# Optimization experiments

Measured on AMD Instinct MI355X. Metric: run time of the kernel, lower is better.

The kernel has to match this reference:

```python
import jax, jax.numpy as jnp
import numpy as np

DIM = 2048
HEADS = 16
HDIM = DIM // HEADS  # 128
B = 1
F, HG, WG = 5, 20, 32
L = F * HG * WG  # 3200
EPS = 1e-6
MAXPOS = 1024
C = HDIM // 2  # 64 rotary pairs
S0 = C - 2 * (C // 3)  # 22 (frame band)
S1 = C // 3            # 21 (height band)


def _rope_tables():
    # Matches Wan rope_params: per-band inverse-freq tables, angle = pos * inv_freq.
    pos = np.arange(MAXPOS, dtype=np.float64)
    chunks = []
    for s in (S0, S1, S1):
        d = 2 * s
        inv = 1.0 / (10000.0 ** (np.arange(0, d, 2, dtype=np.float64) / d))
        chunks.append(np.outer(pos, inv))
    ang = np.concatenate(chunks, axis=1)  # [MAXPOS, C]
    return np.cos(ang).astype(np.float32), np.sin(ang).astype(np.float32)


def setup_inputs() -> dict:
    key = jax.random.key(0)
    ks = jax.random.split(key, 6)
    sc = 1.0 / np.sqrt(DIM)
    fc, fs = _rope_tables()
    return {
        'x': jax.random.normal(ks[0], (B, L, DIM), dtype=jnp.float32),
        'wq': jax.random.normal(ks[1], (DIM, DIM), dtype=jnp.float32) * sc,
        'bq': jnp.zeros((DIM,), jnp.float32),
        'wk': jax.random.normal(ks[2], (DIM, DIM), dtype=jnp.float32) * sc,
        'bk': jnp.zeros((DIM,), jnp.float32),
        'wv': jax.random.normal(ks[3], (DIM, DIM), dtype=jnp.float32) * sc,
        'bv': jnp.zeros((DIM,), jnp.float32),
        'wo': jax.random.normal(ks[4], (DIM, DIM), dtype=jnp.float32) * sc,
        'bo': jnp.zeros((DIM,), jnp.float32),
        'norm_q_w': jnp.ones((DIM,), jnp.float32),
        'norm_k_w': jnp.ones((DIM,), jnp.float32),
        'freqs_cos': jnp.asarray(fc),
        'freqs_sin': jnp.asarray(fs),
    }


def _grid_freqs(tab):
    # Split bands and broadcast over the (F, HG, WG) grid -> [L, C]
    bf, bh, bw = tab[:, :S0], tab[:, S0:S0 + S1], tab[:, S0 + S1:]
    gf = jnp.broadcast_to(bf[:F, None, None, :], (F, HG, WG, S0))
    gh = jnp.broadcast_to(bh[None, :HG, None, :], (F, HG, WG, S1))
    gw = jnp.broadcast_to(bw[None, None, :WG, :], (F, HG, WG, S1))
    return jnp.concatenate([gf, gh, gw], axis=-1).reshape(L, C)


def reference(x, wq, bq, wk, bk, wv, bv, wo, bo, norm_q_w, norm_k_w, freqs_cos, freqs_sin):
    def rms(t, w):
        return t * jax.lax.rsqrt(jnp.mean(t * t, axis=-1, keepdims=True) + EPS) * w

    q = rms(x @ wq.T + bq, norm_q_w).reshape(B, L, HEADS, HDIM)
    k = rms(x @ wk.T + bk, norm_k_w).reshape(B, L, HEADS, HDIM)
    v = (x @ wv.T + bv).reshape(B, L, HEADS, HDIM)

    fc = _grid_freqs(freqs_cos)  # [L, C]
    fs = _grid_freqs(freqs_sin)

    def rope(t):
        tr = t.reshape(B, L, HEADS, C, 2)
        xr, xi = tr[..., 0], tr[..., 1]
        c = fc[None, :, None, :]
        s = fs[None, :, None, :]
        return jnp.stack([xr * c - xi * s, xr * s + xi * c], axis=-1).reshape(B, L, HEADS, HDIM)

    q = rope(q)
    k = rope(k)

    scores = jnp.einsum('blhd,bmhd->bhlm', q, k) / jnp.sqrt(jnp.float32(HDIM))
    attn = jax.nn.softmax(scores, axis=-1)
    out = jnp.einsum('bhlm,bmhd->blhd', attn, v).reshape(B, L, DIM)
    return out @ wo.T + bo
```

## Files before the change

kernel.cpp:

```cpp
#include <hip/hip_runtime.h>

typedef unsigned short u16;
typedef unsigned int u32;
typedef __attribute__((ext_vector_type(4))) float f32x4;
typedef __attribute__((ext_vector_type(8))) short bf16x8;
typedef __attribute__((ext_vector_type(8))) u16 u16x8;
typedef __attribute__((ext_vector_type(4))) u16 u16x4;
typedef __attribute__((ext_vector_type(4))) u32 u32x4;

#define GLOB_AS __attribute__((address_space(1)))
#define LDS_AS  __attribute__((address_space(3)))

__device__ __forceinline__ void gload_lds16(const void* g, void* l) {
  __builtin_amdgcn_global_load_lds((const GLOB_AS void*)g, (LDS_AS void*)l, 16, 0, 0);
}

__device__ __forceinline__ u16 f2bf(float f) {
  u32 u = __builtin_bit_cast(u32, f);
  u += 0x7fffu + ((u >> 16) & 1u);
  return (u16)(u >> 16);
}

__device__ __forceinline__ float bf2f(u16 b) {
  u32 u = (u32)b << 16;
  return __builtin_bit_cast(float, u);
}

#define MFMA16(a, b, c) __builtin_amdgcn_mfma_f32_16x16x32_bf16(a, b, c, 0, 0, 0)

__global__ __launch_bounds__(256) void cast_all(const float* __restrict__ x,
                                                const float* __restrict__ wq,
                                                const float* __restrict__ wk,
                                                const float* __restrict__ wv,
                                                const float* __restrict__ wo,
                                                u16* __restrict__ xb, u16* __restrict__ wqb,
                                                u16* __restrict__ wkb, u16* __restrict__ wvb,
                                                u16* __restrict__ wob) {
  int i = blockIdx.x * 256 + threadIdx.x;
  const float* s;
  u16* d;
  int off;
  if (i < 819200)       { s = x;  d = xb;  off = i; }
  else if (i < 1343488) { s = wq; d = wqb; off = i - 819200; }
  else if (i < 1867776) { s = wk; d = wkb; off = i - 1343488; }
  else if (i < 2392064) { s = wv; d = wvb; off = i - 1867776; }
  else                  { s = wo; d = wob; off = i - 2392064; }
  f32x4 a = ((const f32x4*)s)[2 * off], b = ((const f32x4*)s)[2 * off + 1];
  u16x8 o;
  o[0] = f2bf(a[0]); o[1] = f2bf(a[1]); o[2] = f2bf(a[2]); o[3] = f2bf(a[3]);
  o[4] = f2bf(b[0]); o[5] = f2bf(b[1]); o[6] = f2bf(b[2]); o[7] = f2bf(b[3]);
  ((u16x8*)d)[off] = o;
}

#define GEMM_BODY(C_WRITE)                                                        \
  f32x4 acc[4][4] = {};                                                           \
  const u32 dstoff = wave * 2048 + lane * 8;       \
  int gsb = 0;                                                                    \
  const u16* Agp = Ag;                                                            \
  const u16* Bgp = Bg;                                                            \
  _Pragma("unroll") for (int pf = 0; pf < 2; ++pf) {                              \
    u16* ad = &As[gsb][0] + dstoff;                                               \
    u16* bd = &Bs[gsb][0] + dstoff;                                               \
    gload_lds16(Agp, ad);                                                         \
    gload_lds16(Agp + (size_t)8 * K + d4, ad + 512);                              \
    gload_lds16(Agp + (size_t)16 * K, ad + 1024);                                 \
    gload_lds16(Agp + (size_t)24 * K + d4, ad + 1536);                            \
    gload_lds16(Bgp, bd);                                                         \
    gload_lds16(Bgp + (size_t)8 * K + d4, bd + 512);                              \
    gload_lds16(Bgp + (size_t)16 * K, bd + 1024);                                 \
    gload_lds16(Bgp + (size_t)24 * K + d4, bd + 1536);                            \
    Agp += 64;                                                                    \
    Bgp += 64;                                                                    \
    gsb ^= 1;                                                                     \
  }                                                                               \
  for (int it = 0; it < 32; ++it) {                                               \
    const int buf = it & 1;                                                       \
    if (it < 31)                                                                  \
      asm volatile("s_waitcnt vmcnt(8)" ::: "memory");                            \
    else                                                                          \
      asm volatile("s_waitcnt vmcnt(0)" ::: "memory");                            \
    __builtin_amdgcn_s_barrier();                                                 \
    _Pragma("unroll") for (int kk = 0; kk < 64; kk += 32) {                       \
      bf16x8 af[4], bfr[4];                                                       \
      _Pragma("unroll") for (int mi = 0; mi < 4; mi++)                            \
          af[mi] = *(const bf16x8*)&As[buf][((wr + mi * 16 + li) >> 1) * 128 +    \
              ((((kk >> 3) + lg + 8 * (li & 1)) ^ (li >> 1)) * 8)];               \
      _Pragma("unroll") for (int ni = 0; ni < 4; ni++)                            \
          bfr[ni] = *(const bf16x8*)&Bs[buf][((wc + ni * 16 + li) >> 1) * 128 +   \
              ((((kk >> 3) + lg + 8 * (li & 1)) ^ (li >> 1)) * 8)];               \
      _Pragma("unroll") for (int mi = 0; mi < 4; mi++)                            \
          _Pragma("unroll") for (int ni = 0; ni < 4; ni++)                        \
              acc[mi][ni] = MFMA16(af[mi], bfr[ni], acc[mi][ni]);                 \
    }                                                                             \
    __builtin_amdgcn_s_barrier();                                                 \
    if (it <= 29) {                                                               \
      u16* ad = &As[gsb][0] + dstoff;                                             \
      u16* bd = &Bs[gsb][0] + dstoff;                                             \
      gload_lds16(Agp, ad);                                                       \
      gload_lds16(Agp + (size_t)8 * K + d4, ad + 512);                            \
      gload_lds16(Agp + (size_t)16 * K, ad + 1024);                               \
      gload_lds16(Agp + (size_t)24 * K + d4, ad + 1536);                          \
      gload_lds16(Bgp, bd);                                                       \
      gload_lds16(Bgp + (size_t)8 * K + d4, bd + 512);                            \
      gload_lds16(Bgp + (size_t)16 * K, bd + 1024);                               \
      gload_lds16(Bgp + (size_t)24 * K + d4, bd + 1536);                          \
      Agp += 64;                                                                  \
      Bgp += 64;                                                                  \
      gsb ^= 1;                                                                   \
    }                                                                             \
  }                                                                               \
  float bcol[4];                                                                  \
  _Pragma("unroll") for (int ni = 0; ni < 4; ni++)                                \
      bcol[ni] = bias[n0 + wc + ni * 16 + li];                                    \
  _Pragma("unroll") for (int mi = 0; mi < 4; mi++) {                              \
    _Pragma("unroll") for (int ni = 0; ni < 4; ni++) {                            \
      const int gm = m0 + wr + mi * 16 + lg * 4;                                  \
      const int gn = n0 + wc + ni * 16 + li;                                      \
      _Pragma("unroll") for (int r = 0; r < 4; r++) { C_WRITE; }                  \
    }                                                                             \
  }

#define GEMM_STAGE_SETUP()                                        \
  const int Wl = lane >> 4;                                       \
  const int sl = lane & 15;                                       \
  const int gsa = sl ^ Wl;                                        \
  const int d4 = ((((gsa & 7) ^ 4) - (gsa & 7)) * 8)

__global__ __launch_bounds__(256) void gemm_qkv(const u16* __restrict__ A,
                                                const u16* __restrict__ Bq,
                                                const u16* __restrict__ Bk,
                                                const u16* __restrict__ Bv,
                                                const float* __restrict__ bq,
                                                const float* __restrict__ bk,
                                                const float* __restrict__ bv,
                                                u16* __restrict__ Cq,
                                                u16* __restrict__ Ck,
                                                u16* __restrict__ Cv) {
  constexpr int K = 2048, N = 2048;
  __shared__ u16 As[2][128 * 64];
  __shared__ u16 Bs[2][128 * 64];
  const int tid = threadIdx.x;
  const int wave = tid >> 6, lane = tid & 63;
  const int lg = lane >> 4, li = lane & 15;
  const int lid = blockIdx.x + 25 * blockIdx.y;
  const int tile = (lid & 7) * 150 + (lid >> 3);
  const int bx = tile % 25, by = tile / 25;
  const int m0 = bx * 128;
  const int mat = by >> 4;
  const int n0 = (by & 15) * 128;
  const u16* B = (mat == 0) ? Bq : (mat == 1) ? Bk : Bv;
  const float* bias = (mat == 0) ? bq : (mat == 1) ? bk : bv;
  u16* C = (mat == 0) ? Cq : (mat == 1) ? Ck : Cv;
  const int wr = (wave >> 1) * 64, wc = (wave & 1) * 64;

  GEMM_STAGE_SETUP();
  const u16* Ag = A + (size_t)(m0 + wave * 32 + 2 * Wl + (sl >> 3)) * K + (gsa & 7) * 8;
  const u16* Bg = B + (size_t)(n0 + wave * 32 + 2 * Wl + (sl >> 3)) * K + (gsa & 7) * 8;

  GEMM_BODY(C[(size_t)(gm + r) * N + gn] = f2bf(acc[mi][ni][r] + bcol[ni]))
}

__global__ __launch_bounds__(256) void gemm_nt(const u16* __restrict__ A,
                                               const u16* __restrict__ B,
                                               const float* __restrict__ bias,
                                               float* __restrict__ C) {
  constexpr int K = 2048, N = 2048;
  __shared__ u16 As[2][128 * 64];
  __shared__ u16 Bs[2][128 * 64];
  const int tid = threadIdx.x;
  const int wave = tid >> 6, lane = tid & 63;
  const int lg = lane >> 4, li = lane & 15;
  const int lid = blockIdx.x + 25 * blockIdx.y;
  const int tile = (lid & 7) * 50 + (lid >> 3);
  const int m0 = (tile % 25) * 128, n0 = (tile / 25) * 128;
  const int wr = (wave >> 1) * 64, wc = (wave & 1) * 64;

  GEMM_STAGE_SETUP();
  const u16* Ag = A + (size_t)(m0 + wave * 32 + 2 * Wl + (sl >> 3)) * K + (gsa & 7) * 8;
  const u16* Bg = B + (size_t)(n0 + wave * 32 + 2 * Wl + (sl >> 3)) * K + (gsa & 7) * 8;

  GEMM_BODY(C[(size_t)(gm + r) * N + gn] = acc[mi][ni][r] + bcol[ni])
}

__global__ __launch_bounds__(256) void rms_rope2(const u16* __restrict__ preq,
                                                 const u16* __restrict__ prek,
                                                 const float* __restrict__ wq,
                                                 const float* __restrict__ wk,
                                                 const float* __restrict__ fcos,
                                                 const float* __restrict__ fsin,
                                                 u16* __restrict__ outq,
                                                 u16* __restrict__ outk, float foldq) {
  const int isk = blockIdx.x >= 3200;
  const int l = isk ? blockIdx.x - 3200 : blockIdx.x;
  const u16* pre = isk ? prek : preq;
  const float* w = isk ? wk : wq;
  u16* out = isk ? outk : outq;
  const float fold = isk ? 1.0f : foldq;
  const int tid = threadIdx.x;
  const int d0 = tid * 8;
  u16x8 pv = *(const u16x8*)(pre + (size_t)l * 2048 + d0);
  float xv[8];
#pragma unroll
  for (int j = 0; j < 8; j++) xv[j] = bf2f(pv[j]);
  float ss = (xv[0] * xv[0] + xv[1] * xv[1]) + (xv[2] * xv[2] + xv[3] * xv[3]) +
             (xv[4] * xv[4] + xv[5] * xv[5]) + (xv[6] * xv[6] + xv[7] * xv[7]);
#pragma unroll
  for (int m = 32; m; m >>= 1) ss += __shfl_xor(ss, m);
  __shared__ float red[4];
  if ((tid & 63) == 0) red[tid >> 6] = ss;
  __syncthreads();
  const float scale =
      rsqrtf((red[0] + red[1] + red[2] + red[3]) * (1.0f / 2048.0f) + 1e-6f) * fold;
  f32x4 w0 = *(const f32x4*)(w + d0);
  f32x4 w1 = *(const f32x4*)(w + d0 + 4);
  float xs[8];
#pragma unroll
  for (int j = 0; j < 4; j++) {
    xs[j] = xv[j] * w0[j] * scale;
    xs[4 + j] = xv[4 + j] * w1[j] * scale;
  }
  const int f = l / 640, rem = l % 640;
  const int hh = rem >> 5, ww = rem & 31;
  const int cb = (d0 & 127) >> 1;
  u16x8 ov;
#pragma unroll
  for (int i = 0; i < 4; i++) {
    const int c = cb + i;
    const int prow = c < 22 ? f : (c < 43 ? hh : ww);
    const float fc = fcos[prow * 64 + c];
    const float fs = fsin[prow * 64 + c];
    const float xr = xs[2 * i], xi = xs[2 * i + 1];
    ov[2 * i] = f2bf(xr * fc - xi * fs);
    ov[2 * i + 1] = f2bf(xr * fs + xi * fc);
  }
  *(u16x8*)(out + (size_t)l * 2048 + d0) = ov;
}

__global__ __launch_bounds__(256) void transpose_2d(const u16* __restrict__ src,
                                                    u16* __restrict__ dst) {
  __shared__ u16 t[64][72];
  const int m0 = blockIdx.x * 64, n0 = blockIdx.y * 64;
  const int tid = threadIdx.x;
  const int r = tid >> 3, c8 = (tid & 7) * 8;
#pragma unroll
  for (int j = 0; j < 2; j++) {
    u16x8 v = *(const u16x8*)&src[(size_t)(m0 + r + 32 * j) * 2048 + n0 + c8];
#pragma unroll
    for (int e = 0; e < 8; e++) t[c8 + e][r + 32 * j] = v[e];
  }
  __syncthreads();
  const int b = (c8 >> 5) * 32;
  const int cc = ((c8 >> 3) & 3) * 4;
#pragma unroll
  for (int j = 0; j < 2; j++) {
    const u16* trow = &t[r + 32 * j][0];
    u16x4 lo = *(const u16x4*)&trow[b + cc];
    u16x4 hi = *(const u16x4*)&trow[b + 16 + cc];
    u16x8 v;
    v[0] = lo[0]; v[1] = lo[1]; v[2] = lo[2]; v[3] = lo[3];
    v[4] = hi[0]; v[5] = hi[1]; v[6] = hi[2]; v[7] = hi[3];
    *(u16x8*)&dst[(size_t)(n0 + r + 32 * j) * 3200 + m0 + c8] = v;
  }
}

__global__ __launch_bounds__(512) void attn_kernel(const u16* __restrict__ Q,
                                                   const u16* __restrict__ Kb,
                                                   const u16* __restrict__ VT,
                                                   u16* __restrict__ O) {
  __shared__ u16 Klds[2][64 * 128];
  __shared__ u16 Vlds[2][128 * 64];
  const int tid = threadIdx.x, wave = tid >> 6, lane = tid & 63;
  const int lg = lane >> 4, li = lane & 15;

  const int lid = blockIdx.x + 25 * blockIdx.y;
  const int xcd = lid & 7, ixd = lid >> 3;
  const int h = xcd * 2 + (ixd & 1);
  const int qrow0 = (ixd >> 1) * 128 + wave * 16;

  bf16x8 qf[4];
  {
    const u16* qb = Q + (size_t)(qrow0 + li) * 2048 + h * 128 + lg * 8;
#pragma unroll
    for (int ks = 0; ks < 4; ks++) qf[ks] = *(const bf16x8*)(qb + ks * 32);
  }
  f32x4 o[8] = {};
  float lrow = 0.f;

  const int klp = lane >> 4;
  const int kg0 = (lane & 15) ^ klp;
  const int kd4 = ((kg0 ^ 4) - kg0) * 8;
  const u16* kp = Kb + (size_t)(wave * 8 + klp) * 2048 + h * 128 + kg0 * 8;
  const int vlp = lane >> 3;
  const int vg = (lane & 7) ^ vlp;
  const u16* vp = VT + (size_t)(h * 128 + wave * 16 + vlp) * 3200 + vg * 8;
  const u32 dstoff = wave * 1024 + lane * 8;
  int sb = 0;

#define STAGE()                               \
  do {                                        \
    u16* kd = &Klds[sb][0] + dstoff;          \
    u16* vd = &Vlds[sb][0] + dstoff;          \
    gload_lds16(kp, kd);                      \
    gload_lds16(kp + 4 * 2048 + kd4, kd + 512); \
    gload_lds16(vp, vd);                      \
    gload_lds16(vp + 8 * 3200, vd + 512);     \
    kp += 64 * 2048;                          \
    vp += 64;                                 \
    sb ^= 1;                                  \
  } while (0)

  STAGE();
  STAGE();

  for (int it = 0; it < 50; ++it) {
    const int buf = it & 1;
    if (it < 49)
      asm volatile("s_waitcnt vmcnt(4)" ::: "memory");
    else
      asm volatile("s_waitcnt vmcnt(0)" ::: "memory");
    __builtin_amdgcn_s_barrier();

    f32x4 s4[4] = {};
#pragma unroll
    for (int t = 0; t < 4; t++)
#pragma unroll
      for (int ks = 0; ks < 4; ks++) {
        const bf16x8 kf = *(const bf16x8*)&Klds[buf][(t * 16 + li) * 128 +
                                                     ((ks * 4 + lg) ^ (li & 7)) * 8];
        s4[t] = MFMA16(kf, qf[ks], s4[t]);
      }
    f32x4 p[4];
#pragma unroll
    for (int t = 0; t < 4; t++)
#pragma unroll
      for (int i = 0; i < 4; i++) p[t][i] = exp2f(s4[t][i] - 24.0f);
    lrow += ((p[0][0] + p[0][1]) + (p[0][2] + p[0][3])) +
            ((p[1][0] + p[1][1]) + (p[1][2] + p[1][3])) +
            ((p[2][0] + p[2][1]) + (p[2][2] + p[2][3])) +
            ((p[3][0] + p[3][1]) + (p[3][2] + p[3][3]));
    u32 wp[8];
    asm("v_cvt_pk_bf16_f32 %0, %1, %2" : "=v"(wp[0]) : "v"(p[0][0]), "v"(p[0][1]));
    asm("v_cvt_pk_bf16_f32 %0, %1, %2" : "=v"(wp[1]) : "v"(p[0][2]), "v"(p[0][3]));
    asm("v_cvt_pk_bf16_f32 %0, %1, %2" : "=v"(wp[2]) : "v"(p[1][0]), "v"(p[1][1]));
    asm("v_cvt_pk_bf16_f32 %0, %1, %2" : "=v"(wp[3]) : "v"(p[1][2]), "v"(p[1][3]));
    asm("v_cvt_pk_bf16_f32 %0, %1, %2" : "=v"(wp[4]) : "v"(p[2][0]), "v"(p[2][1]));
    asm("v_cvt_pk_bf16_f32 %0, %1, %2" : "=v"(wp[5]) : "v"(p[2][2]), "v"(p[2][3]));
    asm("v_cvt_pk_bf16_f32 %0, %1, %2" : "=v"(wp[6]) : "v"(p[3][0]), "v"(p[3][1]));
    asm("v_cvt_pk_bf16_f32 %0, %1, %2" : "=v"(wp[7]) : "v"(p[3][2]), "v"(p[3][3]));
    u32x4 paw0 = {wp[0], wp[1], wp[2], wp[3]};
    u32x4 paw1 = {wp[4], wp[5], wp[6], wp[7]};
    const bf16x8 pa0 = __builtin_bit_cast(bf16x8, paw0);
    const bf16x8 pa1 = __builtin_bit_cast(bf16x8, paw1);

#pragma unroll
    for (int tt = 0; tt < 2; tt++)
#pragma unroll
      for (int f8 = 0; f8 < 8; f8++) {
        const bf16x8 vf = *(const bf16x8*)&Vlds[buf][(f8 * 16 + li) * 64 +
                                                     ((tt * 4 + lg) ^ (li & 7)) * 8];
        o[f8] = MFMA16(tt ? pa1 : pa0, vf, o[f8]);
      }
    __builtin_amdgcn_s_barrier();
    if (it <= 47) STAGE();
  }
#undef STAGE

  float lt = lrow;
  lt += __shfl_xor(lt, 16);
  lt += __shfl_xor(lt, 32);
  const float inv = 1.0f / lt;
  float invi[4];
#pragma unroll
  for (int i = 0; i < 4; i++) invi[i] = __shfl(inv, lg * 4 + i);
#pragma unroll
  for (int i = 0; i < 4; i++) {
    const int row = qrow0 + lg * 4 + i;
#pragma unroll
    for (int f8 = 0; f8 < 8; f8++)
      O[(size_t)row * 2048 + h * 128 + f8 * 16 + li] = f2bf(o[f8][i] * invi[i]);
  }
}

extern "C" void kernel_launch(void* const* d_in, const int* in_sizes, int n_in,
                              void* d_out, int out_size, void* d_ws, size_t ws_size,
                              hipStream_t stream) {
  const float* x    = (const float*)d_in[0];
  const float* wq   = (const float*)d_in[1];
  const float* bq   = (const float*)d_in[2];
  const float* wk   = (const float*)d_in[3];
  const float* bk   = (const float*)d_in[4];
  const float* wv   = (const float*)d_in[5];
  const float* bv   = (const float*)d_in[6];
  const float* wo   = (const float*)d_in[7];
  const float* bo   = (const float*)d_in[8];
  const float* nqw  = (const float*)d_in[9];
  const float* nkw  = (const float*)d_in[10];
  const float* fcos = (const float*)d_in[11];
  const float* fsin = (const float*)d_in[12];

  const size_t NEED = 125304832;
  if (ws_size < NEED) return;
  char* ws = (char*)d_ws;
  u16* x_bf   = (u16*)(ws + 0);
  u16* wq_bf  = (u16*)(ws + 13107200);
  u16* wk_bf  = (u16*)(ws + 21495808);
  u16* wv_bf  = (u16*)(ws + 29884416);
  u16* wo_bf  = (u16*)(ws + 38273024);
  u16* preq   = (u16*)(ws + 46661632);
  u16* prek   = (u16*)(ws + 59768832);
  u16* v_bf   = (u16*)(ws + 72876032);
  u16* q_bf   = (u16*)(ws + 85983232);
  u16* k_bf   = (u16*)(ws + 99090432);
  u16* vT     = (u16*)(ws + 112197632);
  u16* att_bf = (u16*)(ws + 46661632);

  cast_all<<<11392, 256, 0, stream>>>(x, wq, wk, wv, wo, x_bf, wq_bf, wk_bf, wv_bf,
                                      wo_bf);

  const float foldq = 1.4426950408889634f * 0.08838834764831843f;

  gemm_qkv<<<dim3(25, 48), 256, 0, stream>>>(x_bf, wq_bf, wk_bf, wv_bf, bq, bk, bv,
                                             preq, prek, v_bf);
  rms_rope2<<<6400, 256, 0, stream>>>(preq, prek, nqw, nkw, fcos, fsin, q_bf, k_bf,
                                      foldq);
  transpose_2d<<<dim3(50, 32), 256, 0, stream>>>(v_bf, vT);
  attn_kernel<<<dim3(25, 16), 512, 0, stream>>>(q_bf, k_bf, vT, att_bf);
  gemm_nt<<<dim3(25, 16), 256, 0, stream>>>(att_bf, wo_bf, bo, (float*)d_out);
}
```

Measured before the change: 313.0 us.

## Split attention KV range in two with persistent atomic work queue and combine pass

Each attention block's key/value range is split into two halves, giving 800 work items. A persistent grid of 512 blocks pulls these items from an atomic counter, which the transpose kernel resets. Partial outputs and row sums are written to workspace, and a new combine kernel merges the halves weighted by their row sums before the output projection. This targets the tail imbalance of the original 400-block grid on 256 CUs. In exchange it adds an extra kernel, extra memory traffic for the bf16 partials, and one more bf16 rounding step. It also reuses workspace regions (x_bf, wq_bf, v_bf) that are dead by this point.

Result: slower. 330.3 us (+5.5%).

```diff
diff --git a/kernel.cpp b/kernel.cpp
--- a/kernel.cpp
+++ b/kernel.cpp
@@ -237,7 +237,9 @@
 }
 
 __global__ __launch_bounds__(256) void transpose_2d(const u16* __restrict__ src,
-                                                    u16* __restrict__ dst) {
+                                                    u16* __restrict__ dst,
+                                                    int* __restrict__ counter) {
+  if (blockIdx.x == 0 && blockIdx.y == 0 && threadIdx.x == 0) *counter = 0;
   __shared__ u16 t[64][72];
   const int m0 = blockIdx.x * 64, n0 = blockIdx.y * 64;
   const int tid = threadIdx.x;
@@ -266,35 +268,45 @@
 __global__ __launch_bounds__(512) void attn_kernel(const u16* __restrict__ Q,
                                                    const u16* __restrict__ Kb,
                                                    const u16* __restrict__ VT,
-                                                   u16* __restrict__ O) {
+                                                   u16* __restrict__ Opart,
+                                                   float* __restrict__ ml,
+                                                   int* __restrict__ counter) {
   __shared__ u16 Klds[2][64 * 128];
   __shared__ u16 Vlds[2][128 * 64];
+  __shared__ int curit;
   const int tid = threadIdx.x, wave = tid >> 6, lane = tid & 63;
   const int lg = lane >> 4, li = lane & 15;
-
-  const int lid = blockIdx.x + 25 * blockIdx.y;
-  const int xcd = lid & 7, ixd = lid >> 3;
-  const int h = xcd * 2 + (ixd & 1);
-  const int qrow0 = (ixd >> 1) * 128 + wave * 16;
-
-  bf16x8 qf[4];
-  {
-    const u16* qb = Q + (size_t)(qrow0 + li) * 2048 + h * 128 + lg * 8;
-#pragma unroll
-    for (int ks = 0; ks < 4; ks++) qf[ks] = *(const bf16x8*)(qb + ks * 32);
-  }
-  f32x4 o[8] = {};
-  float lrow = 0.f;
 
   const int klp = lane >> 4;
   const int kg0 = (lane & 15) ^ klp;
   const int kd4 = ((kg0 ^ 4) - kg0) * 8;
-  const u16* kp = Kb + (size_t)(wave * 8 + klp) * 2048 + h * 128 + kg0 * 8;
   const int vlp = lane >> 3;
   const int vg = (lane & 7) ^ vlp;
-  const u16* vp = VT + (size_t)(h * 128 + wave * 16 + vlp) * 3200 + vg * 8;
   const u32 dstoff = wave * 1024 + lane * 8;
-  int sb = 0;
+
+  for (;;) {
+    if (tid == 0) curit = atomicAdd(counter, 1);
+    __syncthreads();
+    const int item = curit;
+    if (item >= 800) return;
+    const int split = item & 1;
+    const int h = (item >> 1) & 15;
+    const int qt = item >> 5;
+    const int qrow0 = qt * 128 + wave * 16;
+    const int n0 = split * 1600;
+
+    bf16x8 qf[4];
+    {
+      const u16* qb = Q + (size_t)(qrow0 + li) * 2048 + h * 128 + lg * 8;
+#pragma unroll
+      for (int ks = 0; ks < 4; ks++) qf[ks] = *(const bf16x8*)(qb + ks * 32);
+    }
+    f32x4 o[8] = {};
+    float lrow = 0.f;
+
+    const u16* kp = Kb + (size_t)(n0 + wave * 8 + klp) * 2048 + h * 128 + kg0 * 8;
+    const u16* vp = VT + (size_t)(h * 128 + wave * 16 + vlp) * 3200 + n0 + vg * 8;
+    int sb = 0;
 
 #define STAGE()                               \
   do {                                        \
@@ -309,76 +321,100 @@
     sb ^= 1;                                  \
   } while (0)
 
-  STAGE();
-  STAGE();
-
-  for (int it = 0; it < 50; ++it) {
-    const int buf = it & 1;
-    if (it < 49)
-      asm volatile("s_waitcnt vmcnt(4)" ::: "memory");
-    else
-      asm volatile("s_waitcnt vmcnt(0)" ::: "memory");
-    __builtin_amdgcn_s_barrier();
-
-    f32x4 s4[4] = {};
-#pragma unroll
-    for (int t = 0; t < 4; t++)
-#pragma unroll
-      for (int ks = 0; ks < 4; ks++) {
-        const bf16x8 kf = *(const bf16x8*)&Klds[buf][(t * 16 + li) * 128 +
-                                                     ((ks * 4 + lg) ^ (li & 7)) * 8];
-        s4[t] = MFMA16(kf, qf[ks], s4[t]);
-      }
-    f32x4 p[4];
-#pragma unroll
-    for (int t = 0; t < 4; t++)
-#pragma unroll
-      for (int i = 0; i < 4; i++) p[t][i] = exp2f(s4[t][i] - 24.0f);
-    lrow += ((p[0][0] + p[0][1]) + (p[0][2] + p[0][3])) +
-            ((p[1][0] + p[1][1]) + (p[1][2] + p[1][3])) +
-            ((p[2][0] + p[2][1]) + (p[2][2] + p[2][3])) +
-            ((p[3][0] + p[3][1]) + (p[3][2] + p[3][3]));
-    u32 wp[8];
-    asm("v_cvt_pk_bf16_f32 %0, %1, %2" : "=v"(wp[0]) : "v"(p[0][0]), "v"(p[0][1]));
-    asm("v_cvt_pk_bf16_f32 %0, %1, %2" : "=v"(wp[1]) : "v"(p[0][2]), "v"(p[0][3]));
-    asm("v_cvt_pk_bf16_f32 %0, %1, %2" : "=v"(wp[2]) : "v"(p[1][0]), "v"(p[1][1]));
-    asm("v_cvt_pk_bf16_f32 %0, %1, %2" : "=v"(wp[3]) : "v"(p[1][2]), "v"(p[1][3]));
-    asm("v_cvt_pk_bf16_f32 %0, %1, %2" : "=v"(wp[4]) : "v"(p[2][0]), "v"(p[2][1]));
-    asm("v_cvt_pk_bf16_f32 %0, %1, %2" : "=v"(wp[5]) : "v"(p[2][2]), "v"(p[2][3]));
-    asm("v_cvt_pk_bf16_f32 %0, %1, %2" : "=v"(wp[6]) : "v"(p[3][0]), "v"(p[3][1]));
-    asm("v_cvt_pk_bf16_f32 %0, %1, %2" : "=v"(wp[7]) : "v"(p[3][2]), "v"(p[3][3]));
-    u32x4 paw0 = {wp[0], wp[1], wp[2], wp[3]};
-    u32x4 paw1 = {wp[4], wp[5], wp[6], wp[7]};
-    const bf16x8 pa0 = __builtin_bit_cast(bf16x8, paw0);
-    const bf16x8 pa1 = __builtin_bit_cast(bf16x8, paw1);
-
-#pragma unroll
-    for (int tt = 0; tt < 2; tt++)
-#pragma unroll
-      for (int f8 = 0; f8 < 8; f8++) {
-        const bf16x8 vf = *(const bf16x8*)&Vlds[buf][(f8 * 16 + li) * 64 +
-                                                     ((tt * 4 + lg) ^ (li & 7)) * 8];
-        o[f8] = MFMA16(tt ? pa1 : pa0, vf, o[f8]);
-      }
-    __builtin_amdgcn_s_barrier();
-    if (it <= 47) STAGE();
-  }
+    STAGE();
+    STAGE();
+
+    for (int it = 0; it < 25; ++it) {
+      const int buf = it & 1;
+      if (it < 24)
+        asm volatile("s_waitcnt vmcnt(4)" ::: "memory");
+      else
+        asm volatile("s_waitcnt vmcnt(0)" ::: "memory");
+      __builtin_amdgcn_s_barrier();
+
+      f32x4 s4[4] = {};
+#pragma unroll
+      for (int t = 0; t < 4; t++)
+#pragma unroll
+        for (int ks = 0; ks < 4; ks++) {
+          const bf16x8 kf = *(const bf16x8*)&Klds[buf][(t * 16 + li) * 128 +
+                                                       ((ks * 4 + lg) ^ (li & 7)) * 8];
+          s4[t] = MFMA16(kf, qf[ks], s4[t]);
+        }
+      f32x4 p[4];
+#pragma unroll
+      for (int t = 0; t < 4; t++)
+#pragma unroll
+        for (int i = 0; i < 4; i++) p[t][i] = exp2f(s4[t][i] - 24.0f);
+      lrow += ((p[0][0] + p[0][1]) + (p[0][2] + p[0][3])) +
+              ((p[1][0] + p[1][1]) + (p[1][2] + p[1][3])) +
+              ((p[2][0] + p[2][1]) + (p[2][2] + p[2][3])) +
+              ((p[3][0] + p[3][1]) + (p[3][2] + p[3][3]));
+      u32 wp[8];
+      asm("v_cvt_pk_bf16_f32 %0, %1, %2" : "=v"(wp[0]) : "v"(p[0][0]), "v"(p[0][1]));
+      asm("v_cvt_pk_bf16_f32 %0, %1, %2" : "=v"(wp[1]) : "v"(p[0][2]), "v"(p[0][3]));
+      asm("v_cvt_pk_bf16_f32 %0, %1, %2" : "=v"(wp[2]) : "v"(p[1][0]), "v"(p[1][1]));
+      asm("v_cvt_pk_bf16_f32 %0, %1, %2" : "=v"(wp[3]) : "v"(p[1][2]), "v"(p[1][3]));
+      asm("v_cvt_pk_bf16_f32 %0, %1, %2" : "=v"(wp[4]) : "v"(p[2][0]), "v"(p[2][1]));
+      asm("v_cvt_pk_bf16_f32 %0, %1, %2" : "=v"(wp[5]) : "v"(p[2][2]), "v"(p[2][3]));
+      asm("v_cvt_pk_bf16_f32 %0, %1, %2" : "=v"(wp[6]) : "v"(p[3][0]), "v"(p[3][1]));
+      asm("v_cvt_pk_bf16_f32 %0, %1, %2" : "=v"(wp[7]) : "v"(p[3][2]), "v"(p[3][3]));
+      u32x4 paw0 = {wp[0], wp[1], wp[2], wp[3]};
+      u32x4 paw1 = {wp[4], wp[5], wp[6], wp[7]};
+      const bf16x8 pa0 = __builtin_bit_cast(bf16x8, paw0);
+      const bf16x8 pa1 = __builtin_bit_cast(bf16x8, paw1);
+
+#pragma unroll
+      for (int tt = 0; tt < 2; tt++)
+#pragma unroll
+        for (int f8 = 0; f8 < 8; f8++) {
+          const bf16x8 vf = *(const bf16x8*)&Vlds[buf][(f8 * 16 + li) * 64 +
+                                                       ((tt * 4 + lg) ^ (li & 7)) * 8];
+          o[f8] = MFMA16(tt ? pa1 : pa0, vf, o[f8]);
+        }
+      __builtin_amdgcn_s_barrier();
+      if (it <= 22) STAGE();
+    }
 #undef STAGE
 
-  float lt = lrow;
-  lt += __shfl_xor(lt, 16);
-  lt += __shfl_xor(lt, 32);
-  const float inv = 1.0f / lt;
-  float invi[4];
-#pragma unroll
-  for (int i = 0; i < 4; i++) invi[i] = __shfl(inv, lg * 4 + i);
-#pragma unroll
-  for (int i = 0; i < 4; i++) {
-    const int row = qrow0 + lg * 4 + i;
-#pragma unroll
-    for (int f8 = 0; f8 < 8; f8++)
-      O[(size_t)row * 2048 + h * 128 + f8 * 16 + li] = f2bf(o[f8][i] * invi[i]);
-  }
+    float lt = lrow;
+    lt += __shfl_xor(lt, 16);
+    lt += __shfl_xor(lt, 32);
+    const float inv = 1.0f / lt;
+    float invi[4];
+#pragma unroll
+    for (int i = 0; i < 4; i++) invi[i] = __shfl(inv, lg * 4 + i);
+#pragma unroll
+    for (int i = 0; i < 4; i++) {
+      const int row = qrow0 + lg * 4 + i;
+#pragma unroll
+      for (int f8 = 0; f8 < 8; f8++)
+        Opart[(size_t)split * 6553600 + (size_t)row * 2048 + h * 128 + f8 * 16 + li] =
+            f2bf(o[f8][i] * invi[i]);
+    }
+    if (lane < 16) {
+      const int row = qrow0 + li;
+      ml[(size_t)(split * 16 + h) * 3200 + row] = lt;
+    }
+  }
+}
+
+__global__ __launch_bounds__(256) void attn_combine(const u16* __restrict__ op,
+                                                    const float* __restrict__ ml,
+                                                    u16* __restrict__ out) {
+  const int row = blockIdx.x, tid = threadIdx.x;
+  const int c8 = tid * 8, h = c8 >> 7;
+  const float l0 = ml[(size_t)h * 3200 + row];
+  const float l1 = ml[(size_t)(16 + h) * 3200 + row];
+  const float inv = 1.0f / (l0 + l1);
+  const float w0 = l0 * inv, w1 = l1 * inv;
+  u16x8 a = *(const u16x8*)&op[(size_t)row * 2048 + c8];
+  u16x8 b = *(const u16x8*)&op[6553600 + (size_t)row * 2048 + c8];
+  u16x8 r;
+#pragma unroll
+  for (int j = 0; j < 8; j++)
+    r[j] = f2bf(bf2f(a[j]) * w0 + bf2f(b[j]) * w1);
+  *(u16x8*)&out[(size_t)row * 2048 + c8] = r;
 }
 
 extern "C" void kernel_launch(void* const* d_in, const int* in_sizes, int n_in,
@@ -412,7 +448,10 @@
   u16* q_bf   = (u16*)(ws + 85983232);
   u16* k_bf   = (u16*)(ws + 99090432);
   u16* vT     = (u16*)(ws + 112197632);
-  u16* att_bf = (u16*)(ws + 46661632);
+  u16* opart  = (u16*)(ws + 46661632);
+  float* ml   = (float*)(ws + 0);
+  int* counter= (int*)(ws + 13107200);
+  u16* att_bf = (u16*)(ws + 72876032);
 
   cast_all<<<11392, 256, 0, stream>>>(x, wq, wk, wv, wo, x_bf, wq_bf, wk_bf, wv_bf,
                                       wo_bf);
@@ -423,7 +462,8 @@
                                              preq, prek, v_bf);
   rms_rope2<<<6400, 256, 0, stream>>>(preq, prek, nqw, nkw, fcos, fsin, q_bf, k_bf,
                                       foldq);
-  transpose_2d<<<dim3(50, 32), 256, 0, stream>>>(v_bf, vT);
-  attn_kernel<<<dim3(25, 16), 512, 0, stream>>>(q_bf, k_bf, vT, att_bf);
+  transpose_2d<<<dim3(50, 32), 256, 0, stream>>>(v_bf, vT, counter);
+  attn_kernel<<<512, 512, 0, stream>>>(q_bf, k_bf, vT, opart, ml, counter);
+  attn_combine<<<3200, 256, 0, stream>>>(opart, ml, att_bf);
   gemm_nt<<<dim3(25, 16), 256, 0, stream>>>(att_bf, wo_bf, bo, (float*)d_out);
 }
```
